# Kernel tuning notes

Measured on AMD Instinct MI355X. Metric: run time of the kernel, lower is better.

Reference implementation:

```python
import jax, jax.numpy as jnp
import numpy as np


def setup_inputs() -> dict:
    key = jax.random.key(0)
    k1, k2 = jax.random.split(key)
    z = jax.random.normal(k1, (16, 128, 32, 32), dtype=jnp.float32)
    codes = jax.random.normal(k2, (8, 512, 16), dtype=jnp.float32)  # [latent_dim, num_codes, channel_dim]
    return {"z": z, "codes": codes}


def reference(z, codes):
    L, K, D = codes.shape          # latent_dim, num_codes, channel_dim
    B, C, H, W = z.shape           # C == L * D
    # permute to channels-last and split channels into (L, D)
    h = jnp.transpose(z, (0, 2, 3, 1)).reshape(B, H, W, L, D)
    # pairwise L2 distances via ||h||^2 - 2 h.W + ||W||^2 (avoids materializing [B,H,W,L,K,D])
    h2 = jnp.sum(h * h, axis=-1)                      # [B,H,W,L]
    w2 = jnp.sum(codes * codes, axis=-1)              # [L,K]
    cross = jnp.einsum('bhwld,lkd->bhwlk', h, codes)  # [B,H,W,L,K]
    d2 = h2[..., None] - 2.0 * cross + w2[None, None, None]
    distances = jnp.sqrt(jnp.maximum(d2, 1e-12))      # [B,H,W,L,K]
    # softmin over codes == softmax of negated distances
    probs = jax.nn.softmax(-distances, axis=4)
    soft_symbols = jnp.einsum('bhwlk,lkd->bhwld', probs, codes).reshape(B, H, W, C)
    # hard assignment: nearest code per latent dim
    idxes = jnp.argmin(distances, axis=4)             # [B,H,W,L]
    hard_symbols = codes[jnp.arange(L), idxes]        # [B,H,W,L,D]
    hard_symbols = hard_symbols.reshape(B, H, W, C)
    return (soft_symbols, hard_symbols, idxes)
```

## Files before the change

kernel.cpp:

```cpp
#include <hip/hip_runtime.h>
#include <hip/hip_bf16.h>

typedef float  f32x4  __attribute__((ext_vector_type(4)));
typedef short  s16x8  __attribute__((ext_vector_type(8)));
typedef __bf16 bf16x8 __attribute__((ext_vector_type(8)));
typedef unsigned int u32x2 __attribute__((ext_vector_type(2)));
typedef unsigned int u32x4 __attribute__((ext_vector_type(4)));

namespace {
constexpr int BHW = 16384, L = 8, K = 512, D = 16, HW = 1024, CH = 128;
constexpr int TPB = 512;
constexpr int PPB = 128;
constexpr size_t WS_CA_ELEMS = (size_t)L * K * 32;
constexpr size_t WS_NEED = WS_CA_ELEMS * 2 + (size_t)L * K * 4;

__device__ __forceinline__ f32x4 mfma16(s16x8 a, s16x8 b, f32x4 c) {
  return __builtin_amdgcn_mfma_f32_16x16x32_bf16(
      __builtin_bit_cast(bf16x8, a), __builtin_bit_cast(bf16x8, b), c, 0, 0, 0);
}
__device__ __forceinline__ unsigned short bfh(float x) {
  return __builtin_bit_cast(unsigned short, __float2bfloat16(x));
}
__device__ __forceinline__ float bf2f(unsigned short u) {
  return __bfloat162float(__builtin_bit_cast(__hip_bfloat16, u));
}

__global__ void repack(const float* __restrict__ codes,
                       unsigned short* __restrict__ cA, float* __restrict__ w2g) {
  int i = blockIdx.x * 256 + threadIdx.x;
  const float* c = codes + (size_t)i * D;
  float s = 0.f;
  #pragma unroll
  for (int d = 0; d < D; ++d) s = fmaf(c[d], c[d], s);
  w2g[i] = s;
  unsigned short* dst = cA + (size_t)i * 32;
  #pragma unroll
  for (int d = 0; d < D; ++d) {
    unsigned short hi = bfh(c[d]);
    unsigned short lo = bfh(c[d] - bf2f(hi));
    dst[d] = hi; dst[16 + d] = lo;
  }
}

__global__ __launch_bounds__(TPB, 4) void enc_mfma(
    const float* __restrict__ z,
    const float* __restrict__ codes,
    const unsigned short* __restrict__ cA,
    const float* __restrict__ w2g,
    float* __restrict__ out)
{
  __shared__ unsigned short cH[512 * 18];
  __shared__ unsigned short cL[512 * 18];
  __shared__ float w2s[512];
  __shared__ unsigned short Pl[8][16][32];
  __shared__ unsigned short hH[128][16];
  __shared__ unsigned short hL[128][16];
  __shared__ float h2s[128];
  __shared__ float ssum[8][16];
  __shared__ int   bks[8][16];

  const int tid  = threadIdx.x;
  const int l    = blockIdx.y;
  const int bx   = blockIdx.x;
  const int bimg = bx >> 3;
  const int yx0  = (bx & 7) * 128;

  float* hstg = (float*)cH;
  {
    const int i = tid & 127, dc = tid >> 7;
    #pragma unroll
    for (int it = 0; it < 4; ++it) {
      int d = dc + it * 4;
      hstg[i * 17 + d] = z[((size_t)(bimg * CH + l * D + d)) * HW + yx0 + i];
    }
  }
  __syncthreads();
  if (tid < 128) {
    float h[16]; float h2 = 0.f;
    #pragma unroll
    for (int d = 0; d < 16; ++d) h[d] = hstg[tid * 17 + d];
    #pragma unroll
    for (int d = 0; d < 16; ++d) h2 = fmaf(h[d], h[d], h2);
    h2s[tid] = h2;
    #pragma unroll
    for (int d = 0; d < 16; ++d) {
      unsigned short hi = bfh(h[d]);
      hH[tid][d] = hi;
      hL[tid][d] = bfh(h[d] - bf2f(hi));
    }
  }
  __syncthreads();
  {
    const unsigned short* src = cA + ((size_t)l * K + tid) * 32;
    #pragma unroll
    for (int d = 0; d < 16; ++d) { cH[tid * 18 + d] = src[d]; cL[tid * 18 + d] = src[16 + d]; }
    w2s[tid] = w2g[l * K + tid];
  }
  __syncthreads();

  const int wv   = __builtin_amdgcn_readfirstlane(tid >> 6);
  const int lane = tid & 63;
  const int cl   = lane & 15;
  const int g    = lane >> 4;
  const int pw   = wv * 16;
  const int myp  = pw + cl;

  s16x8 B1 = *(const s16x8*)&hH[myp][(g & 1) * 8];
  s16x8 B2 = *(const s16x8*)&hL[myp][(g & 1) * 8];
  const float h2 = h2s[myp];

  const s16x8* Ab = (const s16x8*)(cA + (size_t)l * K * 32) + (cl * 4 + g);

  char* Pb = (char*)&Pl[wv][0][0] + cl * 64;
  const int w0off = ((g    ) ^ (cl & 7)) << 3;
  const int w1off = ((4 + g) ^ (cl & 7)) << 3;
  const int r0off = ((2 * g    ) ^ (cl & 7)) << 3;
  const int r1off = ((2 * g + 1) ^ (cl & 7)) << 3;

  float m2k = 1e30f, m2bk = 1e30f, s = 0.f;
  f32x4 pv = {0.f, 0.f, 0.f, 0.f};

  #pragma unroll 4
  for (int ck = 0; ck < 16; ++ck) {
    s16x8 A0 = Ab[ck * 128];
    s16x8 A1 = Ab[ck * 128 + 64];
    f32x4 T0 = {0.f, 0.f, 0.f, 0.f}, T1 = {0.f, 0.f, 0.f, 0.f};
    T0 = mfma16(A0, B1, T0); T0 = mfma16(A0, B2, T0);
    T1 = mfma16(A1, B1, T1); T1 = mfma16(A1, B2, T1);

    f32x4 W0 = *(const f32x4*)&w2s[ck * 32 + g * 4];
    f32x4 W1 = *(const f32x4*)&w2s[ck * 32 + 16 + g * 4];

    float wt[8];
    #pragma unroll
    for (int t = 0; t < 2; ++t) {
      #pragma unroll
      for (int r = 0; r < 4; ++r) {
        float T  = t ? T1[r] : T0[r];
        float Wk = t ? W1[r] : W0[r];
        float d2 = fmaf(-2.f, T, h2) + Wk;
        d2 = fmaxf(d2, 1e-12f);
        int kloc = ck * 32 + t * 16 + g * 4 + r;
        float key = __int_as_float((__float_as_int(d2) & 0xFFFFFE00) | kloc);
        m2bk = __builtin_amdgcn_fmed3f(key, m2k, m2bk);
        m2k  = fminf(m2k, key);
        float dist = __builtin_amdgcn_sqrtf(d2);
        float w = __builtin_amdgcn_exp2f(dist * -1.44269504088896340736f);
        s += w;
        wt[t * 4 + r] = w;
      }
    }
    #pragma unroll
    for (int t = 0; t < 2; ++t) {
      unsigned p01 = (unsigned)bfh(wt[t*4+0]) | ((unsigned)bfh(wt[t*4+1]) << 16);
      unsigned p23 = (unsigned)bfh(wt[t*4+2]) | ((unsigned)bfh(wt[t*4+3]) << 16);
      *(unsigned*)(Pb + (t ? w1off : w0off) + 0) = p01;
      *(unsigned*)(Pb + (t ? w1off : w0off) + 4) = p23;
    }
    u32x2 pa0 = *(const u32x2*)(Pb + r0off);
    u32x2 pa1 = *(const u32x2*)(Pb + r1off);
    u32x4 pau; pau[0] = pa0[0]; pau[1] = pa0[1]; pau[2] = pa1[0]; pau[3] = pa1[1];
    s16x8 PA = __builtin_bit_cast(s16x8, pau);
    s16x8 Bh, Bl;
    #pragma unroll
    for (int j = 0; j < 8; ++j) {
      Bh[j] = (short)cH[(ck * 32 + 8 * g + j) * 18 + cl];
      Bl[j] = (short)cL[(ck * 32 + 8 * g + j) * 18 + cl];
    }
    pv = mfma16(PA, Bh, pv);
    pv = mfma16(PA, Bl, pv);
  }

  #pragma unroll
  for (int off = 16; off < 64; off <<= 1) {
    s += __shfl_xor(s, off);
    float m2o  = __shfl_xor(m2k, off);
    float m2bo = __shfl_xor(m2bk, off);
    m2bk = fminf(fminf(m2bk, m2bo), fmaxf(m2k, m2o));
    m2k  = fminf(m2k, m2o);
  }
  int ka = __float_as_int(m2k) & 511;
  float d2min = __int_as_float(__float_as_int(m2k)  & 0xFFFFFE00);
  float d2sec = __int_as_float(__float_as_int(m2bk) & 0xFFFFFE00);
  bool trig = (d2sec - d2min) < 0.02f;

  if (lane < 16) { ssum[wv][lane] = s; bks[wv][lane] = ka; }

  unsigned long long mask = __ballot(lane < 16 && trig);
  while (mask) {
    int pl = __ffsll((long long)mask) - 1; mask &= mask - 1;
    float hh[16];
    #pragma unroll
    for (int d = 0; d < 16; ++d)
      hh[d] = z[((size_t)(bimg * CH + l * D + d)) * HW + yx0 + pw + pl];
    float h2x = h2s[pw + pl];
    float bm = 1e30f; int bkk = 0;
    for (int rnd = 0; rnd < 8; ++rnd) {
      int k = rnd * 64 + lane;
      const float* cr = codes + ((size_t)l * K + k) * D;
      float cross = 0.f;
      #pragma unroll
      for (int d = 0; d < 16; ++d) cross = fmaf(hh[d], cr[d], cross);
      float d2 = (h2x - 2.f * cross) + w2g[l * K + k];
      d2 = fmaxf(d2, 1e-12f);
      float dist = sqrtf(d2);
      if (dist < bm) { bm = dist; bkk = k; }
    }
    #pragma unroll
    for (int off = 1; off < 64; off <<= 1) {
      float bo = __shfl_xor(bm, off); int ko = __shfl_xor(bkk, off);
      if (bo < bm || (bo == bm && ko < bkk)) { bm = bo; bkk = ko; }
    }
    if (lane == 0) bks[wv][pl] = bkk;
  }

  const int pg0 = bimg * HW + yx0;
  f32x4 sv = *(const f32x4*)&ssum[wv][g * 4];
  #pragma unroll
  for (int r = 0; r < 4; ++r) {
    float inv = __builtin_amdgcn_rcpf(sv[r]);
    out[(size_t)(pg0 + pw + g * 4 + r) * CH + l * D + cl] = pv[r] * inv;
  }
  int kk = bks[wv][cl];
  float4 cv = *(const float4*)&codes[((size_t)l * K + kk) * D + g * 4];
  *(float4*)&out[(size_t)BHW * CH + (size_t)(pg0 + pw + cl) * CH + l * D + g * 4] = cv;
  if (lane < 16)
    out[(size_t)2 * BHW * CH + (size_t)(pg0 + pw + cl) * L + l] = (float)kk;
}
}

extern "C" void kernel_launch(void* const* d_in, const int* in_sizes, int n_in,
                              void* d_out, int out_size, void* d_ws, size_t ws_size,
                              hipStream_t stream) {
  const float* z     = (const float*)d_in[0];
  const float* codes = (const float*)d_in[1];
  float* out         = (float*)d_out;
  unsigned short* cA = (unsigned short*)d_ws;
  float* w2g         = (float*)((char*)d_ws + WS_CA_ELEMS * 2);

  repack<<<dim3(L * K / 256), 256, 0, stream>>>(codes, cA, w2g);
  dim3 grid(BHW / PPB, L);
  enc_mfma<<<grid, TPB, 0, stream>>>(z, codes, cA, w2g, out);
}
```

Measured before the change: 72.17 us.

## Permute code rows so softmax weights feed MFMA directly without LDS round-trip

The repack kernel now stores code rows in a permuted order, so each lane's eight softmax weights already sit in the operand layout the second MFMA expects. That removes the per-iteration write and read of the probability tile through shared memory. The B operands for the weighted sum are pre-transposed into LDS so each lane reads them with one vector load instead of eight scalar loads. Two independent accumulators are used for the hi and lo parts, the unroll factor drops to 2, and launch bounds are raised to five blocks per CU, which adds register pressure.

```diff
diff --git a/kernel.cpp b/kernel.cpp
--- a/kernel.cpp
+++ b/kernel.cpp
@@ -4,15 +4,12 @@
 typedef float  f32x4  __attribute__((ext_vector_type(4)));
 typedef short  s16x8  __attribute__((ext_vector_type(8)));
 typedef __bf16 bf16x8 __attribute__((ext_vector_type(8)));
-typedef unsigned int u32x2 __attribute__((ext_vector_type(2)));
-typedef unsigned int u32x4 __attribute__((ext_vector_type(4)));
 
 namespace {
 constexpr int BHW = 16384, L = 8, K = 512, D = 16, HW = 1024, CH = 128;
 constexpr int TPB = 512;
 constexpr int PPB = 128;
 constexpr size_t WS_CA_ELEMS = (size_t)L * K * 32;
-constexpr size_t WS_NEED = WS_CA_ELEMS * 2 + (size_t)L * K * 4;
 
 __device__ __forceinline__ f32x4 mfma16(s16x8 a, s16x8 b, f32x4 c) {
   return __builtin_amdgcn_mfma_f32_16x16x32_bf16(
@@ -33,28 +30,28 @@
   #pragma unroll
   for (int d = 0; d < D; ++d) s = fmaf(c[d], c[d], s);
   w2g[i] = s;
-  unsigned short* dst = cA + (size_t)i * 32;
+  int l = i >> 9, k = i & (K - 1);
+  int ck = k >> 5, kloc = k & 31, g = kloc >> 3, w = kloc & 7, t = w >> 2, r = w & 3;
+  int prow = ck * 32 + t * 16 + g * 4 + r;
+  unsigned short* dst = cA + ((size_t)l * K + prow) * 32;
   #pragma unroll
   for (int d = 0; d < D; ++d) {
     unsigned short hi = bfh(c[d]);
-    unsigned short lo = bfh(c[d] - bf2f(hi));
-    dst[d] = hi; dst[16 + d] = lo;
-  }
-}
-
-__global__ __launch_bounds__(TPB, 4) void enc_mfma(
+    dst[d] = hi; dst[16 + d] = bfh(c[d] - bf2f(hi));
+  }
+}
+
+__global__ __launch_bounds__(TPB, 5) void enc_mfma(
     const float* __restrict__ z,
     const float* __restrict__ codes,
     const unsigned short* __restrict__ cA,
     const float* __restrict__ w2g,
     float* __restrict__ out)
 {
-  __shared__ unsigned short cH[512 * 18];
-  __shared__ unsigned short cL[512 * 18];
-  __shared__ float w2s[512];
-  __shared__ unsigned short Pl[8][16][32];
-  __shared__ unsigned short hH[128][16];
-  __shared__ unsigned short hL[128][16];
+  __shared__ unsigned short cBh[8192];
+  __shared__ unsigned short cBl[8192];
+  __shared__ float w2s[K];
+  __shared__ unsigned short hH[128][16], hL[128][16];
   __shared__ float h2s[128];
   __shared__ float ssum[8][16];
   __shared__ int   bks[8][16];
@@ -65,7 +62,7 @@
   const int bimg = bx >> 3;
   const int yx0  = (bx & 7) * 128;
 
-  float* hstg = (float*)cH;
+  float* hstg = (float*)cBh;
   {
     const int i = tid & 127, dc = tid >> 7;
     #pragma unroll
@@ -91,10 +88,19 @@
   }
   __syncthreads();
   {
-    const unsigned short* src = cA + ((size_t)l * K + tid) * 32;
-    #pragma unroll
-    for (int d = 0; d < 16; ++d) { cH[tid * 18 + d] = src[d]; cL[tid * 18 + d] = src[16 + d]; }
-    w2s[tid] = w2g[l * K + tid];
+    int k = tid, ck = k >> 5, kloc = k & 31, g = kloc >> 3, w = kloc & 7, t = w >> 2, r = w & 3;
+    int prow = ck * 32 + t * 16 + g * 4 + r;
+    const s16x8* src = (const s16x8*)(cA + ((size_t)l * K + prow) * 32);
+    s16x8 h0 = src[0], h1 = src[1], l0 = src[2], l1 = src[3];
+    int base = (ck * 4 + g) * 128 + w;
+    #pragma unroll
+    for (int d = 0; d < 8; ++d) {
+      cBh[base + d * 8]       = (unsigned short)h0[d];
+      cBl[base + d * 8]       = (unsigned short)l0[d];
+      cBh[base + (d + 8) * 8] = (unsigned short)h1[d];
+      cBl[base + (d + 8) * 8] = (unsigned short)l1[d];
+    }
+    w2s[k] = w2g[l * K + k];
   }
   __syncthreads();
 
@@ -111,25 +117,22 @@
 
   const s16x8* Ab = (const s16x8*)(cA + (size_t)l * K * 32) + (cl * 4 + g);
 
-  char* Pb = (char*)&Pl[wv][0][0] + cl * 64;
-  const int w0off = ((g    ) ^ (cl & 7)) << 3;
-  const int w1off = ((4 + g) ^ (cl & 7)) << 3;
-  const int r0off = ((2 * g    ) ^ (cl & 7)) << 3;
-  const int r1off = ((2 * g + 1) ^ (cl & 7)) << 3;
-
   float m2k = 1e30f, m2bk = 1e30f, s = 0.f;
-  f32x4 pv = {0.f, 0.f, 0.f, 0.f};
-
-  #pragma unroll 4
+  f32x4 pv0 = {0.f, 0.f, 0.f, 0.f}, pv1 = {0.f, 0.f, 0.f, 0.f};
+
+  #pragma unroll 2
   for (int ck = 0; ck < 16; ++ck) {
     s16x8 A0 = Ab[ck * 128];
     s16x8 A1 = Ab[ck * 128 + 64];
+    s16x8 Bh = *(const s16x8*)&cBh[(ck * 4 + g) * 128 + cl * 8];
+    s16x8 Bl = *(const s16x8*)&cBl[(ck * 4 + g) * 128 + cl * 8];
+
     f32x4 T0 = {0.f, 0.f, 0.f, 0.f}, T1 = {0.f, 0.f, 0.f, 0.f};
     T0 = mfma16(A0, B1, T0); T0 = mfma16(A0, B2, T0);
     T1 = mfma16(A1, B1, T1); T1 = mfma16(A1, B2, T1);
 
-    f32x4 W0 = *(const f32x4*)&w2s[ck * 32 + g * 4];
-    f32x4 W1 = *(const f32x4*)&w2s[ck * 32 + 16 + g * 4];
+    f32x4 W0 = *(const f32x4*)&w2s[ck * 32 + 8 * g];
+    f32x4 W1 = *(const f32x4*)&w2s[ck * 32 + 8 * g + 4];
 
     float wt[8];
     #pragma unroll
@@ -140,7 +143,7 @@
         float Wk = t ? W1[r] : W0[r];
         float d2 = fmaf(-2.f, T, h2) + Wk;
         d2 = fmaxf(d2, 1e-12f);
-        int kloc = ck * 32 + t * 16 + g * 4 + r;
+        int kloc = ck * 32 + 8 * g + t * 4 + r;
         float key = __int_as_float((__float_as_int(d2) & 0xFFFFFE00) | kloc);
         m2bk = __builtin_amdgcn_fmed3f(key, m2k, m2bk);
         m2k  = fminf(m2k, key);
@@ -150,26 +153,13 @@
         wt[t * 4 + r] = w;
       }
     }
-    #pragma unroll
-    for (int t = 0; t < 2; ++t) {
-      unsigned p01 = (unsigned)bfh(wt[t*4+0]) | ((unsigned)bfh(wt[t*4+1]) << 16);
-      unsigned p23 = (unsigned)bfh(wt[t*4+2]) | ((unsigned)bfh(wt[t*4+3]) << 16);
-      *(unsigned*)(Pb + (t ? w1off : w0off) + 0) = p01;
-      *(unsigned*)(Pb + (t ? w1off : w0off) + 4) = p23;
-    }
-    u32x2 pa0 = *(const u32x2*)(Pb + r0off);
-    u32x2 pa1 = *(const u32x2*)(Pb + r1off);
-    u32x4 pau; pau[0] = pa0[0]; pau[1] = pa0[1]; pau[2] = pa1[0]; pau[3] = pa1[1];
-    s16x8 PA = __builtin_bit_cast(s16x8, pau);
-    s16x8 Bh, Bl;
-    #pragma unroll
-    for (int j = 0; j < 8; ++j) {
-      Bh[j] = (short)cH[(ck * 32 + 8 * g + j) * 18 + cl];
-      Bl[j] = (short)cL[(ck * 32 + 8 * g + j) * 18 + cl];
-    }
-    pv = mfma16(PA, Bh, pv);
-    pv = mfma16(PA, Bl, pv);
-  }
+    s16x8 PA;
+    #pragma unroll
+    for (int j = 0; j < 8; ++j) PA[j] = (short)bfh(wt[j]);
+    pv0 = mfma16(PA, Bh, pv0);
+    pv1 = mfma16(PA, Bl, pv1);
+  }
+  f32x4 pv = pv0 + pv1;
 
   #pragma unroll
   for (int off = 16; off < 64; off <<= 1) {
```

Measured after the change: 73.43 us. No clear change (+1.7%).
